# Performance work log

Measured on AMD Instinct MI355X. Metric: run time of the kernel, lower is better.

The kernel has to match this reference:

```python
import jax, jax.numpy as jnp
import numpy as np

PATCH_SIZE = 16  # init_kwargs patch_size


def setup_inputs() -> dict:
    key = jax.random.key(0)
    k1, k2, k3 = jax.random.split(key, 3)
    B, C, H, W = 128, 3, 224, 224
    n_points = int(H * W * 0.5 / PATCH_SIZE ** 2)  # 98
    imgs = jax.random.normal(k1, (B, C, H, W), dtype=jnp.float32)
    points_x = jax.random.randint(k2, (B, n_points), 0, H - PATCH_SIZE + 1, dtype=jnp.int32)
    points_y = jax.random.randint(k3, (B, n_points), 0, W - PATCH_SIZE + 1, dtype=jnp.int32)
    return {"imgs": imgs, "points_x": points_x, "points_y": points_y}


def reference(imgs, points_x, points_y):
    # imgs: [B, C, H, W]; points_x/points_y: [B, N] top-left corners of P x P patches to zero.
    B, C, H, W = imgs.shape
    P = PATCH_SIZE
    off = jnp.arange(P, dtype=points_x.dtype)
    b = jnp.arange(B)[:, None, None, None]                       # [B,1,1,1]
    xs = points_x[:, :, None, None] + off[None, None, :, None]    # [B,N,P,1]
    ys = points_y[:, :, None, None] + off[None, None, None, :]    # [B,N,1,P]
    # Build occlusion mask once with a single scatter, then apply across channels.
    mask = jnp.zeros((B, H, W), dtype=jnp.bool_).at[b, xs, ys].set(True)  # [B,H,W]
    return jnp.where(mask[:, None, :, :], jnp.zeros((), imgs.dtype), imgs)
```

## Files before the change

### kernel.cpp

```cpp
#include <hip/hip_runtime.h>

#define BB 128
#define CC 3
#define HH 224
#define WW 224
#define PP 16

#define W4 (WW / 4)
#define CHAN4 (HH * W4)
#define PER_IMG4 (CC * CHAN4)
#define TOTAL4 (BB * PER_IMG4)
#define NROWS 6

typedef float vfloat4 __attribute__((ext_vector_type(4)));

__global__ __launch_bounds__(256) void occl_fused(
        vfloat4* __restrict__ out, const vfloat4* __restrict__ imgs,
        const int* __restrict__ px, const int* __restrict__ py, int N) {
    const int t = threadIdx.x;
    const int blockF0 = blockIdx.x * 256;
    const int f = blockF0 + t;

    const int b       = blockF0 / PER_IMG4;
    const int localF0 = blockF0 % CHAN4;
    const int h0      = localF0 / W4;

    __shared__ unsigned int rowbits[NROWS * 7];

    if (t < NROWS * 7) rowbits[t] = 0u;

    vfloat4 v = imgs[f];

    __syncthreads();

    if (t < N) {
        int x = px[b * N + t];
        int y = py[b * N + t];
        int lo = x > h0 ? x : h0;
        int hi = (x + PP < h0 + NROWS) ? (x + PP) : (h0 + NROWS);
        if (lo < hi) {
            unsigned long long mm = 0xFFFFull << (y & 31);
            unsigned int lo32 = (unsigned int)mm;
            unsigned int hi32 = (unsigned int)(mm >> 32);
            int woff = y >> 5;
            for (int h = lo; h < hi; ++h) {
                int base = (h - h0) * 7 + woff;
                atomicOr(&rowbits[base], lo32);
                if (hi32) atomicOr(&rowbits[base + 1], hi32);
            }
        }
    }
    __syncthreads();

    int lf = localF0 + t;
    int w4 = lf % W4;
    int h  = lf / W4;
    unsigned int word = rowbits[(h - h0) * 7 + (w4 >> 3)];
    unsigned int m4 = (word >> ((w4 & 7) * 4)) & 0xFu;
    if (m4 & 1u) v.x = 0.f;
    if (m4 & 2u) v.y = 0.f;
    if (m4 & 4u) v.z = 0.f;
    if (m4 & 8u) v.w = 0.f;
    __builtin_nontemporal_store(v, &out[f]);
}

extern "C" void kernel_launch(void* const* d_in, const int* in_sizes, int n_in,
                              void* d_out, int out_size, void* d_ws, size_t ws_size,
                              hipStream_t stream) {
    const float* imgs = (const float*)d_in[0];
    const int*   px   = (const int*)d_in[1];
    const int*   py   = (const int*)d_in[2];
    float*       out  = (float*)d_out;

    const int N = in_sizes[1] / BB;

    occl_fused<<<TOTAL4 / 256, 256, 0, stream>>>(
        (vfloat4*)out, (const vfloat4*)imgs, px, py, N);
}
```

Baseline: 137.7 us.

## Process all three channels per thread and skip loads for fully masked pixels

Each block now covers one spatial tile of an image and handles all three channels, so the patch-mask bitmap is built once per tile rather than once per channel. Loads of pixel groups that are fully occluded are skipped, and the remaining loads are nontemporal. The image load now happens after the mask build instead of overlapping it, which may expose latency, and each thread has more work while the grid is a third of its former size.

```diff
diff --git a/kernel.cpp b/kernel.cpp
--- a/kernel.cpp
+++ b/kernel.cpp
@@ -9,28 +9,21 @@
 #define W4 (WW / 4)
 #define CHAN4 (HH * W4)
 #define PER_IMG4 (CC * CHAN4)
-#define TOTAL4 (BB * PER_IMG4)
 #define NROWS 6
+#define NBLK (BB * (CHAN4 / 256))
 
 typedef float vfloat4 __attribute__((ext_vector_type(4)));
 
 __global__ __launch_bounds__(256) void occl_fused(
         vfloat4* __restrict__ out, const vfloat4* __restrict__ imgs,
         const int* __restrict__ px, const int* __restrict__ py, int N) {
-    const int t = threadIdx.x;
-    const int blockF0 = blockIdx.x * 256;
-    const int f = blockF0 + t;
-
-    const int b       = blockF0 / PER_IMG4;
-    const int localF0 = blockF0 % CHAN4;
-    const int h0      = localF0 / W4;
+    const int t     = threadIdx.x;
+    const int b     = blockIdx.x / (CHAN4 / 256);
+    const int posF0 = (blockIdx.x % (CHAN4 / 256)) * 256;
+    const int h0    = posF0 / W4;
 
     __shared__ unsigned int rowbits[NROWS * 7];
-
     if (t < NROWS * 7) rowbits[t] = 0u;
-
-    vfloat4 v = imgs[f];
-
     __syncthreads();
 
     if (t < N) {
@@ -52,16 +45,27 @@
     }
     __syncthreads();
 
-    int lf = localF0 + t;
-    int w4 = lf % W4;
-    int h  = lf / W4;
+    int p  = posF0 + t;
+    int w4 = p % W4;
+    int h  = p / W4;
     unsigned int word = rowbits[(h - h0) * 7 + (w4 >> 3)];
     unsigned int m4 = (word >> ((w4 & 7) * 4)) & 0xFu;
-    if (m4 & 1u) v.x = 0.f;
-    if (m4 & 2u) v.y = 0.f;
-    if (m4 & 4u) v.z = 0.f;
-    if (m4 & 8u) v.w = 0.f;
-    __builtin_nontemporal_store(v, &out[f]);
+
+    size_t f0 = (size_t)b * PER_IMG4 + p;
+    vfloat4 z = {0.f, 0.f, 0.f, 0.f};
+    vfloat4 v0 = z, v1 = z, v2 = z;
+    if (m4 != 0xFu) {
+        v0 = __builtin_nontemporal_load(&imgs[f0]);
+        v1 = __builtin_nontemporal_load(&imgs[f0 + CHAN4]);
+        v2 = __builtin_nontemporal_load(&imgs[f0 + 2 * CHAN4]);
+        if (m4 & 1u) { v0.x = 0.f; v1.x = 0.f; v2.x = 0.f; }
+        if (m4 & 2u) { v0.y = 0.f; v1.y = 0.f; v2.y = 0.f; }
+        if (m4 & 4u) { v0.z = 0.f; v1.z = 0.f; v2.z = 0.f; }
+        if (m4 & 8u) { v0.w = 0.f; v1.w = 0.f; v2.w = 0.f; }
+    }
+    __builtin_nontemporal_store(v0, &out[f0]);
+    __builtin_nontemporal_store(v1, &out[f0 + CHAN4]);
+    __builtin_nontemporal_store(v2, &out[f0 + 2 * CHAN4]);
 }
 
 extern "C" void kernel_launch(void* const* d_in, const int* in_sizes, int n_in,
@@ -74,6 +78,6 @@
 
     const int N = in_sizes[1] / BB;
 
-    occl_fused<<<TOTAL4 / 256, 256, 0, stream>>>(
+    occl_fused<<<NBLK, 256, 0, stream>>>(
         (vfloat4*)out, (const vfloat4*)imgs, px, py, N);
 }
```

Result: faster. 134.6 us (-2.2%).
